# Kernel tuning notes

Measured on AMD Instinct MI355X. Metric: run time of the kernel, lower is better.

Reference implementation:

```python
import jax, jax.numpy as jnp
import numpy as np

HID = 1024
HEADS = 16
HEAD_DIM = HID // HEADS


def setup_inputs() -> dict:
    key = jax.random.key(0)
    ks = jax.random.split(key, 12)
    B, S = 4, 2048
    scale = 0.02
    return {
        "query": jax.random.normal(ks[0], (B, S, HID), jnp.float32),
        "key": jax.random.normal(ks[1], (B, S, HID), jnp.float32),
        "value": jax.random.normal(ks[2], (B, S, HID), jnp.float32),
        "wq": jax.random.normal(ks[3], (HID, HID), jnp.float32) * scale,
        "bq": jnp.zeros((HID,), jnp.float32),
        "wk": jax.random.normal(ks[4], (HID, HID), jnp.float32) * scale,
        "bk": jnp.zeros((HID,), jnp.float32),
        "wv": jax.random.normal(ks[5], (HID, HID), jnp.float32) * scale,
        "bv": jnp.zeros((HID,), jnp.float32),
        "wf": jax.random.normal(ks[6], (HID, HID), jnp.float32) * scale,
        "bf": jnp.zeros((HID,), jnp.float32),
    }


def reference(query, key, value, wq, bq, wk, bk, wv, bv, wf, bf):
    B, S, _ = query.shape
    # torch Linear: y = x @ W.T + b
    Q = (query @ wq.T + bq).reshape(B, S, HEADS, HEAD_DIM).transpose(0, 2, 1, 3)
    K = (key @ wk.T + bk).reshape(B, S, HEADS, HEAD_DIM).transpose(0, 2, 1, 3)
    V = (value @ wv.T + bv).reshape(B, S, HEADS, HEAD_DIM).transpose(0, 2, 1, 3)
    scale = jnp.sqrt(jnp.float32(HEAD_DIM))
    energy = jnp.einsum('bhqd,bhkd->bhqk', Q, K) / scale  # [B,H,S,S]
    attention = jax.nn.softmax(energy, axis=-1)  # dropout p=0 -> identity
    x = jnp.einsum('bhqk,bhkd->bhqd', attention, V)
    x = x.transpose(0, 2, 1, 3).reshape(B, S, HID)
    return x @ wf.T + bf
```

## Files before the change

kernel.cpp:

```cpp
#include <hip/hip_runtime.h>
#include <stdint.h>

#define SEQ 2048
#define HIDDEN 1024
#define NHEADS 16
#define HDIM 64
#define MTOT 8192

#define C1SCALE 0.1803368801111437f

typedef __bf16 bf16x8 __attribute__((ext_vector_type(8)));
typedef unsigned short u16x8 __attribute__((ext_vector_type(8)));
typedef short s16x4 __attribute__((ext_vector_type(4)));
typedef unsigned int u32x4 __attribute__((ext_vector_type(4)));
typedef float f32x4 __attribute__((ext_vector_type(4)));

#define GAS __attribute__((address_space(1)))
#define LAS __attribute__((address_space(3)))

__device__ __forceinline__ unsigned short bf16_rne(float f) {
  union { float f; unsigned int u; } v; v.f = f;
  return (unsigned short)((v.u + 0x7fffu + ((v.u >> 16) & 1u)) >> 16);
}

__device__ __forceinline__ unsigned int pk2(float lo, float hi) {
  unsigned int a = __builtin_bit_cast(unsigned int, hi) + 0x8000u;
  unsigned int b = __builtin_bit_cast(unsigned int, lo) + 0x8000u;
  return __builtin_amdgcn_perm(a, b, 0x07060302u);
}

__device__ __forceinline__ s16x4 pack4_bf16(float a, float b, float c, float d) {
  s16x4 r;
  r[0] = (short)bf16_rne(a); r[1] = (short)bf16_rne(b);
  r[2] = (short)bf16_rne(c); r[3] = (short)bf16_rne(d);
  return r;
}

__device__ __forceinline__ void gload_lds16(const unsigned short* g, unsigned short* l) {
  __builtin_amdgcn_global_load_lds((GAS void*)(unsigned short*)g, (LAS void*)l, 16, 0, 0);
}

__global__ __launch_bounds__(256) void cvt3(const float* __restrict__ a,
                                            const float* __restrict__ b,
                                            const float* __restrict__ c,
                                            unsigned short* __restrict__ out,
                                            int perSeg) {
  const int seg = blockIdx.y;
  const float* in = seg == 0 ? a : (seg == 1 ? b : c);
  int i = blockIdx.x * 256 + threadIdx.x;
  float4 v = ((const float4*)in)[i];
  ushort4 o;
  o.x = bf16_rne(v.x); o.y = bf16_rne(v.y);
  o.z = bf16_rne(v.z); o.w = bf16_rne(v.w);
  ((ushort4*)(out + (size_t)seg * perSeg))[i] = o;
}

__global__ __launch_bounds__(256) void cvt4(const float* __restrict__ a,
                                            const float* __restrict__ b,
                                            const float* __restrict__ c,
                                            const float* __restrict__ d,
                                            unsigned short* __restrict__ out,
                                            int perSeg) {
  const int seg = blockIdx.y;
  const float* in = seg == 0 ? a : (seg == 1 ? b : (seg == 2 ? c : d));
  const float sc = (seg == 0) ? C1SCALE : 1.0f;
  int i = blockIdx.x * 256 + threadIdx.x;
  float4 v = ((const float4*)in)[i];
  ushort4 o;
  o.x = bf16_rne(v.x * sc); o.y = bf16_rne(v.y * sc);
  o.z = bf16_rne(v.z * sc); o.w = bf16_rne(v.w * sc);
  ((ushort4*)(out + (size_t)seg * perSeg))[i] = o;
}

__global__ __launch_bounds__(256) void gemm_qkv(const unsigned short* __restrict__ Xq,
                                                const unsigned short* __restrict__ Xk,
                                                const unsigned short* __restrict__ Xv,
                                                const unsigned short* __restrict__ W,
                                                const float* __restrict__ bq,
                                                const float* __restrict__ bk,
                                                const float* __restrict__ bv,
                                                unsigned short* __restrict__ Qb,
                                                unsigned short* __restrict__ Kb,
                                                unsigned short* __restrict__ Vb) {
  __shared__ unsigned short As[128 * 32];
  __shared__ unsigned short Bs[128 * 32];
  const int tid = threadIdx.x;
  const int lane = tid & 63, w = tid >> 6;
  const int quad = lane >> 4, ln = lane & 15;
  const int wm = w & 1, wn = w >> 1;
  const int mBase = blockIdx.y * 128, nBase = blockIdx.x * 128;
  const int seg = blockIdx.x >> 3;
  const unsigned short* A = seg == 0 ? Xq : (seg == 1 ? Xk : Xv);
  const float* bias = seg == 0 ? bq : (seg == 1 ? bk : bv);
  const float bscale = seg == 0 ? C1SCALE : 1.0f;
  unsigned short* outp = seg == 0 ? Qb : (seg == 1 ? Kb : Vb);
  const int K = HIDDEN;

  f32x4 acc[4][4];
  f32x4 zero = {0.f, 0.f, 0.f, 0.f};
#pragma unroll
  for (int i = 0; i < 4; i++)
#pragma unroll
    for (int j = 0; j < 4; j++) acc[i][j] = zero;

  const int e0 = tid * 8;
  const int e1 = (256 + tid) * 8;
  const int r0 = e0 >> 5, c0 = e0 & 31;
  const int r1 = e1 >> 5, c1 = e1 & 31;
  const unsigned short* Ap0 = A + (size_t)(mBase + r0) * K + c0;
  const unsigned short* Ap1 = A + (size_t)(mBase + r1) * K + c1;
  const unsigned short* Wp0 = W + (size_t)(nBase + r0) * K + c0;
  const unsigned short* Wp1 = W + (size_t)(nBase + r1) * K + c1;

  for (int k0 = 0; k0 < K; k0 += 32) {
    gload_lds16(Ap0 + k0, &As[e0]);
    gload_lds16(Ap1 + k0, &As[e1]);
    gload_lds16(Wp0 + k0, &Bs[e0]);
    gload_lds16(Wp1 + k0, &Bs[e1]);
    __syncthreads();
    u16x8 af[4], bfr[4];
#pragma unroll
    for (int mi = 0; mi < 4; mi++)
      af[mi] = *(const u16x8*)&As[(wm * 64 + mi * 16 + ln) * 32 + quad * 8];
#pragma unroll
    for (int ni = 0; ni < 4; ni++)
      bfr[ni] = *(const u16x8*)&Bs[(wn * 64 + ni * 16 + ln) * 32 + quad * 8];
#pragma unroll
    for (int mi = 0; mi < 4; mi++)
#pragma unroll
      for (int ni = 0; ni < 4; ni++)
        acc[mi][ni] = __builtin_amdgcn_mfma_f32_16x16x32_bf16(
            __builtin_bit_cast(bf16x8, af[mi]), __builtin_bit_cast(bf16x8, bfr[ni]),
            acc[mi][ni], 0, 0, 0);
    __syncthreads();
  }

#pragma unroll
  for (int ni = 0; ni < 4; ni++) {
    const int colg = nBase + wn * 64 + ni * 16 + ln;
    const int col = colg & 1023;
    const float bvv = bias[col] * bscale;
#pragma unroll
    for (int mi = 0; mi < 4; mi++) {
      const int row = mBase + wm * 64 + mi * 16 + quad * 4;
#pragma unroll
      for (int r = 0; r < 4; r++)
        outp[(size_t)(row + r) * HIDDEN + col] = bf16_rne(acc[mi][ni][r] + bvv);
    }
  }
}

__global__ __launch_bounds__(256) void gemm_f(const unsigned short* __restrict__ A,
                                              const unsigned short* __restrict__ W,
                                              const float* __restrict__ bias,
                                              float* __restrict__ Cv) {
  __shared__ unsigned short As[128 * 32];
  __shared__ unsigned short Bs[128 * 32];
  const int tid = threadIdx.x;
  const int lane = tid & 63, w = tid >> 6;
  const int quad = lane >> 4, ln = lane & 15;
  const int wm = w & 1, wn = w >> 1;
  const int mBase = blockIdx.y * 128, nBase = blockIdx.x * 128;
  const int K = HIDDEN, N = HIDDEN;

  f32x4 acc[4][4];
  f32x4 zero = {0.f, 0.f, 0.f, 0.f};
#pragma unroll
  for (int i = 0; i < 4; i++)
#pragma unroll
    for (int j = 0; j < 4; j++) acc[i][j] = zero;

  const int e0 = tid * 8;
  const int e1 = (256 + tid) * 8;
  const int r0 = e0 >> 5, c0 = e0 & 31;
  const int r1 = e1 >> 5, c1 = e1 & 31;
  const unsigned short* Ap0 = A + (size_t)(mBase + r0) * K + c0;
  const unsigned short* Ap1 = A + (size_t)(mBase + r1) * K + c1;
  const unsigned short* Wp0 = W + (size_t)(nBase + r0) * K + c0;
  const unsigned short* Wp1 = W + (size_t)(nBase + r1) * K + c1;

  for (int k0 = 0; k0 < K; k0 += 32) {
    gload_lds16(Ap0 + k0, &As[e0]);
    gload_lds16(Ap1 + k0, &As[e1]);
    gload_lds16(Wp0 + k0, &Bs[e0]);
    gload_lds16(Wp1 + k0, &Bs[e1]);
    __syncthreads();
    u16x8 af[4], bfr[4];
#pragma unroll
    for (int mi = 0; mi < 4; mi++)
      af[mi] = *(const u16x8*)&As[(wm * 64 + mi * 16 + ln) * 32 + quad * 8];
#pragma unroll
    for (int ni = 0; ni < 4; ni++)
      bfr[ni] = *(const u16x8*)&Bs[(wn * 64 + ni * 16 + ln) * 32 + quad * 8];
#pragma unroll
    for (int mi = 0; mi < 4; mi++)
#pragma unroll
      for (int ni = 0; ni < 4; ni++)
        acc[mi][ni] = __builtin_amdgcn_mfma_f32_16x16x32_bf16(
            __builtin_bit_cast(bf16x8, af[mi]), __builtin_bit_cast(bf16x8, bfr[ni]),
            acc[mi][ni], 0, 0, 0);
    __syncthreads();
  }

#pragma unroll
  for (int ni = 0; ni < 4; ni++) {
    const int col = nBase + wn * 64 + ni * 16 + ln;
    const float bvv = bias[col];
#pragma unroll
    for (int mi = 0; mi < 4; mi++) {
      const int row = mBase + wm * 64 + mi * 16 + quad * 4;
#pragma unroll
      for (int r = 0; r < 4; r++)
        Cv[(size_t)(row + r) * N + col] = acc[mi][ni][r] + bvv;
    }
  }
}

__global__ __launch_bounds__(256) void transpose_v(const unsigned short* __restrict__ Vb,
                                                   unsigned short* __restrict__ Vt) {
  __shared__ unsigned short L[128 * 88];
  const int t = blockIdx.x;
  const int bh = t >> 4, kt = t & 15;
  const int b = bh >> 4, h = bh & 15;
  const int tid = threadIdx.x;
  {
    const int key = tid >> 1, hf = tid & 1;
    const unsigned short* src =
        Vb + ((size_t)(b * SEQ + kt * 128 + key)) * HIDDEN + h * HDIM + hf * 32;
    u16x8 a0 = *(const u16x8*)(src);
    u16x8 a1 = *(const u16x8*)(src + 8);
    u16x8 a2 = *(const u16x8*)(src + 16);
    u16x8 a3 = *(const u16x8*)(src + 24);
    unsigned short* dst = &L[key * 88 + hf * 32];
    *(u16x8*)(dst) = a0;
    *(u16x8*)(dst + 8) = a1;
    *(u16x8*)(dst + 16) = a2;
    *(u16x8*)(dst + 24) = a3;
  }
  __syncthreads();
  const int d = tid & 63, w = tid >> 6;
  unsigned short* out = Vt + (size_t)t * (64 * 128);
#pragma unroll
  for (int gg = 0; gg < 4; gg++) {
    const int G = w * 4 + gg;
    const int g = G >> 2, Phi = G & 3;
    u16x8 v;
#pragma unroll
    for (int j = 0; j < 8; j++) {
      const int kk = g * 32 + (j >> 2) * 16 + Phi * 4 + (j & 3);
      v[j] = L[kk * 88 + d];
    }
    *(u16x8*)(out + d * 128 + ((G ^ (d & 15)) * 8)) = v;
  }
}

__global__ __launch_bounds__(256, 3) void attn5(const unsigned short* __restrict__ Q,
                                                const unsigned short* __restrict__ K,
                                                const unsigned short* __restrict__ Vt,
                                                unsigned short* __restrict__ X) {
  __shared__ unsigned short VtL[2][64 * 128];
  const int tid = threadIdx.x, lane = tid & 63, w = tid >> 6;
  const int quad = lane >> 4, ln = lane & 15;
  const int bh = blockIdx.x, b = bh >> 4, h = bh & 15;
  const size_t base = (size_t)b * SEQ * HIDDEN + (size_t)h * HDIM;
  const unsigned short* Qh = Q + base;
  const unsigned short* Kh = K + base;
  const int qw = blockIdx.y * 128 + w * 32;

  u16x8 qf[2][2];
#pragma unroll
  for (int nt = 0; nt < 2; nt++)
#pragma unroll
    for (int kk2 = 0; kk2 < 2; kk2++)
      qf[nt][kk2] = *(const u16x8*)(Qh + (size_t)(qw + nt * 16 + ln) * HIDDEN + kk2 * 32 + quad * 8);

  f32x4 o[4][2];
  f32x4 zero = {0.f, 0.f, 0.f, 0.f};
#pragma unroll
  for (int mtd = 0; mtd < 4; mtd++)
#pragma unroll
    for (int nt = 0; nt < 2; nt++) o[mtd][nt] = zero;
  f32x4 lacc[2] = {zero, zero};

  const unsigned short* vsrc = Vt + (size_t)bh * 16 * (64 * 128);
  const int ldsOff = w * 2048 + lane * 8;
  const unsigned short* Kl = Kh + (size_t)ln * HIDDEN + quad * 8;

  u16x8 kp[4][2];
#pragma unroll
  for (int m = 0; m < 4; m++) {
    const size_t koff = (size_t)(m * 16) * HIDDEN;
    kp[m][0] = *(const u16x8*)(Kl + koff);
    kp[m][1] = *(const u16x8*)(Kl + koff + 32);
  }
#pragma unroll
  for (int i = 0; i < 4; i++)
    gload_lds16(vsrc + ldsOff + i * 512, &VtL[0][ldsOff + i * 512]);

  for (int kt = 0; kt < 16; ++kt) {
    __syncthreads();
    if (kt < 15) {
      const unsigned short* nsrc = vsrc + (size_t)(kt + 1) * (64 * 128);
      unsigned short* nbuf = &VtL[(kt + 1) & 1][0];
#pragma unroll
      for (int i = 0; i < 4; i++)
        gload_lds16(nsrc + ldsOff + i * 512, &nbuf[ldsOff + i * 512]);
    }
    const unsigned short* vb = &VtL[kt & 1][0];
#pragma unroll
    for (int g = 0; g < 4; g++) {
      u32x4 P[2];
#pragma unroll
      for (int half = 0; half < 2; half++) {
        const int mt = 2 * g + half;
        const int slot = mt & 3;
        f32x4 s0 = zero, s1 = zero;
        s0 = __builtin_amdgcn_mfma_f32_16x16x32_bf16(
            __builtin_bit_cast(bf16x8, kp[slot][0]), __builtin_bit_cast(bf16x8, qf[0][0]), s0, 0, 0, 0);
        s0 = __builtin_amdgcn_mfma_f32_16x16x32_bf16(
            __builtin_bit_cast(bf16x8, kp[slot][1]), __builtin_bit_cast(bf16x8, qf[0][1]), s0, 0, 0, 0);
        s1 = __builtin_amdgcn_mfma_f32_16x16x32_bf16(
            __builtin_bit_cast(bf16x8, kp[slot][0]), __builtin_bit_cast(bf16x8, qf[1][0]), s1, 0, 0, 0);
        s1 = __builtin_amdgcn_mfma_f32_16x16x32_bf16(
            __builtin_bit_cast(bf16x8, kp[slot][1]), __builtin_bit_cast(bf16x8, qf[1][1]), s1, 0, 0, 0);
        if (mt < 4) {
          const size_t koff = ((size_t)(kt * 128 + (mt + 4) * 16)) * HIDDEN;
          kp[slot][0] = *(const u16x8*)(Kl + koff);
          kp[slot][1] = *(const u16x8*)(Kl + koff + 32);
        } else if (kt < 15) {
          const size_t koff = ((size_t)((kt + 1) * 128 + (mt - 4) * 16)) * HIDDEN;
          kp[slot][0] = *(const u16x8*)(Kl + koff);
          kp[slot][1] = *(const u16x8*)(Kl + koff + 32);
        }
        float e0[4], e1[4];
#pragma unroll
        for (int r = 0; r < 4; r++) {
          e0[r] = __builtin_exp2f(s0[r]);
          e1[r] = __builtin_exp2f(s1[r]);
          lacc[0][r] += e0[r];
          lacc[1][r] += e1[r];
        }
        if (half == 0) {
          P[0][0] = pk2(e0[0], e0[1]); P[0][1] = pk2(e0[2], e0[3]);
          P[1][0] = pk2(e1[0], e1[1]); P[1][1] = pk2(e1[2], e1[3]);
        } else {
          P[0][2] = pk2(e0[0], e0[1]); P[0][3] = pk2(e0[2], e0[3]);
          P[1][2] = pk2(e1[0], e1[1]); P[1][3] = pk2(e1[2], e1[3]);
        }
      }
      u16x8 vf[4];
#pragma unroll
      for (int mtd = 0; mtd < 4; mtd++)
        vf[mtd] = *(const u16x8*)&vb[(mtd * 16 + ln) * 128 + (((g * 4 + quad) ^ ln) * 8)];
#pragma unroll
      for (int nt = 0; nt < 2; nt++) {
        bf16x8 pb = __builtin_bit_cast(bf16x8, P[nt]);
#pragma unroll
        for (int mtd = 0; mtd < 4; mtd++)
          o[mtd][nt] = __builtin_amdgcn_mfma_f32_16x16x32_bf16(
              __builtin_bit_cast(bf16x8, vf[mtd]), pb, o[mtd][nt], 0, 0, 0);
      }
    }
  }

  float inv[2];
#pragma unroll
  for (int nt = 0; nt < 2; nt++) {
    float l = lacc[nt][0] + lacc[nt][1] + lacc[nt][2] + lacc[nt][3];
    l += __shfl_xor(l, 16);
    l += __shfl_xor(l, 32);
    inv[nt] = 1.0f / l;
  }
#pragma unroll
  for (int nt = 0; nt < 2; nt++) {
    unsigned short* dst = X + (size_t)(b * SEQ + qw + nt * 16 + ln) * HIDDEN + h * HDIM;
#pragma unroll
    for (int mtd = 0; mtd < 4; mtd++) {
      s16x4 ov = pack4_bf16(o[mtd][nt][0] * inv[nt], o[mtd][nt][1] * inv[nt],
                            o[mtd][nt][2] * inv[nt], o[mtd][nt][3] * inv[nt]);
      *(s16x4*)(dst + mtd * 16 + quad * 4) = ov;
    }
  }
}

extern "C" void kernel_launch(void* const* d_in, const int* in_sizes, int n_in,
                              void* d_out, int out_size, void* d_ws, size_t ws_size,
                              hipStream_t stream) {
  const float* q_in = (const float*)d_in[0];
  const float* k_in = (const float*)d_in[1];
  const float* v_in = (const float*)d_in[2];
  const float* wq = (const float*)d_in[3];
  const float* bq = (const float*)d_in[4];
  const float* wk = (const float*)d_in[5];
  const float* bk = (const float*)d_in[6];
  const float* wv = (const float*)d_in[7];
  const float* bv = (const float*)d_in[8];
  const float* wf = (const float*)d_in[9];
  const float* bfb = (const float*)d_in[10];

  const size_t NX = (size_t)MTOT * HIDDEN;
  const size_t NW = (size_t)HIDDEN * HIDDEN;
  unsigned short* A = (unsigned short*)d_ws;
  unsigned short* Bx = A + NX;
  unsigned short* C = Bx + NX;
  unsigned short* W4 = C + NX;
  unsigned short* Qb = W4 + 4 * NW;
  unsigned short* Kb = Qb + NX;
  unsigned short* Vb = Kb + NX;

  cvt3<<<dim3(NX / 1024, 3), 256, 0, stream>>>(q_in, k_in, v_in, A, (int)NX);
  cvt4<<<dim3(NW / 1024, 4), 256, 0, stream>>>(wq, wk, wv, wf, W4, (int)NW);

  gemm_qkv<<<dim3(24, MTOT / 128), 256, 0, stream>>>(A, Bx, C, W4, bq, bk, bv, Qb, Kb, Vb);
  transpose_v<<<1024, 256, 0, stream>>>(Vb, Bx);
  attn5<<<dim3(NHEADS * 4, SEQ / 128), 256, 0, stream>>>(Qb, Kb, Bx, C);
  gemm_f<<<dim3(8, MTOT / 128), 256, 0, stream>>>(C, W4 + 3 * NW, bfb, (float*)d_out);
}
```

Measured before the change: 411.6 us.

## Pre-swizzle V into MFMA fragment order and load directly from global in attention

The transpose kernel now writes V in exact per-lane MFMA fragment order, so the attention kernel loads V operands straight from global memory and drops the LDS double buffer and its per-tile barriers. The row-sum of exponentials is computed by an extra MFMA against a ones vector instead of VALU adds and cross-lane shuffles. The K prefetch depth is cut from four slots to two, occupancy hint is raised to 4 blocks, and s_setprio brackets the MFMA sections. This trades LDS traffic and synchronisation for more global/L2 loads and one extra MFMA per group.

```diff
diff --git a/kernel.cpp b/kernel.cpp
--- a/kernel.cpp
+++ b/kernel.cpp
@@ -218,7 +218,7 @@
 
 __global__ __launch_bounds__(256) void transpose_v(const unsigned short* __restrict__ Vb,
                                                    unsigned short* __restrict__ Vt) {
-  __shared__ unsigned short L[128 * 88];
+  __shared__ unsigned short L[128 * 90];
   const int t = blockIdx.x;
   const int bh = t >> 4, kt = t & 15;
   const int b = bh >> 4, h = bh & 15;
@@ -231,40 +231,41 @@
     u16x8 a1 = *(const u16x8*)(src + 8);
     u16x8 a2 = *(const u16x8*)(src + 16);
     u16x8 a3 = *(const u16x8*)(src + 24);
-    unsigned short* dst = &L[key * 88 + hf * 32];
+    unsigned short* dst = &L[key * 90 + hf * 32];
     *(u16x8*)(dst) = a0;
     *(u16x8*)(dst + 8) = a1;
     *(u16x8*)(dst + 16) = a2;
     *(u16x8*)(dst + 24) = a3;
   }
   __syncthreads();
-  const int d = tid & 63, w = tid >> 6;
-  unsigned short* out = Vt + (size_t)t * (64 * 128);
+  const int lane = tid & 63, w = tid >> 6;
+  const int quad = lane >> 4, ln = lane & 15;
+  unsigned short* out = Vt + (size_t)t * 8192;
 #pragma unroll
   for (int gg = 0; gg < 4; gg++) {
-    const int G = w * 4 + gg;
-    const int g = G >> 2, Phi = G & 3;
+    const int f = w * 4 + gg;
+    const int g = f >> 2, mtd = f & 3;
     u16x8 v;
 #pragma unroll
     for (int j = 0; j < 8; j++) {
-      const int kk = g * 32 + (j >> 2) * 16 + Phi * 4 + (j & 3);
-      v[j] = L[kk * 88 + d];
+      const int key = g * 32 + (j >> 2) * 16 + quad * 4 + (j & 3);
+      v[j] = L[key * 90 + mtd * 16 + ln];
     }
-    *(u16x8*)(out + d * 128 + ((G ^ (d & 15)) * 8)) = v;
-  }
-}
-
-__global__ __launch_bounds__(256, 3) void attn5(const unsigned short* __restrict__ Q,
+    *(u16x8*)(out + f * 512 + lane * 8) = v;
+  }
+}
+
+__global__ __launch_bounds__(256, 4) void attn6(const unsigned short* __restrict__ Q,
                                                 const unsigned short* __restrict__ K,
                                                 const unsigned short* __restrict__ Vt,
                                                 unsigned short* __restrict__ X) {
-  __shared__ unsigned short VtL[2][64 * 128];
   const int tid = threadIdx.x, lane = tid & 63, w = tid >> 6;
   const int quad = lane >> 4, ln = lane & 15;
   const int bh = blockIdx.x, b = bh >> 4, h = bh & 15;
   const size_t base = (size_t)b * SEQ * HIDDEN + (size_t)h * HDIM;
   const unsigned short* Qh = Q + base;
   const unsigned short* Kh = K + base;
+  const unsigned short* vtile = Vt + (size_t)bh * 16 * 8192;
   const int qw = blockIdx.y * 128 + w * 32;
 
   u16x8 qf[2][2];
@@ -280,41 +281,35 @@
   for (int mtd = 0; mtd < 4; mtd++)
 #pragma unroll
     for (int nt = 0; nt < 2; nt++) o[mtd][nt] = zero;
-  f32x4 lacc[2] = {zero, zero};
-
-  const unsigned short* vsrc = Vt + (size_t)bh * 16 * (64 * 128);
-  const int ldsOff = w * 2048 + lane * 8;
+  f32x4 l2[2] = {zero, zero};
+
+  u16x8 onesf;
+#pragma unroll
+  for (int j = 0; j < 8; j++) onesf[j] = 0x3F80;
+
   const unsigned short* Kl = Kh + (size_t)ln * HIDDEN + quad * 8;
 
-  u16x8 kp[4][2];
-#pragma unroll
-  for (int m = 0; m < 4; m++) {
-    const size_t koff = (size_t)(m * 16) * HIDDEN;
-    kp[m][0] = *(const u16x8*)(Kl + koff);
-    kp[m][1] = *(const u16x8*)(Kl + koff + 32);
-  }
-#pragma unroll
-  for (int i = 0; i < 4; i++)
-    gload_lds16(vsrc + ldsOff + i * 512, &VtL[0][ldsOff + i * 512]);
+  u16x8 kp[2][2];
+  kp[0][0] = *(const u16x8*)(Kl);
+  kp[0][1] = *(const u16x8*)(Kl + 32);
+  kp[1][0] = *(const u16x8*)(Kl + 16 * HIDDEN);
+  kp[1][1] = *(const u16x8*)(Kl + 16 * HIDDEN + 32);
 
   for (int kt = 0; kt < 16; ++kt) {
-    __syncthreads();
-    if (kt < 15) {
-      const unsigned short* nsrc = vsrc + (size_t)(kt + 1) * (64 * 128);
-      unsigned short* nbuf = &VtL[(kt + 1) & 1][0];
-#pragma unroll
-      for (int i = 0; i < 4; i++)
-        gload_lds16(nsrc + ldsOff + i * 512, &nbuf[ldsOff + i * 512]);
-    }
-    const unsigned short* vb = &VtL[kt & 1][0];
 #pragma unroll
     for (int g = 0; g < 4; g++) {
+      u16x8 vp[4];
+#pragma unroll
+      for (int mtd = 0; mtd < 4; mtd++)
+        vp[mtd] = *(const u16x8*)(vtile + kt * 8192 + (g * 4 + mtd) * 512 + lane * 8);
+
       u32x4 P[2];
 #pragma unroll
       for (int half = 0; half < 2; half++) {
         const int mt = 2 * g + half;
-        const int slot = mt & 3;
+        const int slot = mt & 1;
         f32x4 s0 = zero, s1 = zero;
+        __builtin_amdgcn_s_setprio(1);
         s0 = __builtin_amdgcn_mfma_f32_16x16x32_bf16(
             __builtin_bit_cast(bf16x8, kp[slot][0]), __builtin_bit_cast(bf16x8, qf[0][0]), s0, 0, 0, 0);
         s0 = __builtin_amdgcn_mfma_f32_16x16x32_bf16(
@@ -323,22 +318,18 @@
             __builtin_bit_cast(bf16x8, kp[slot][0]), __builtin_bit_cast(bf16x8, qf[1][0]), s1, 0, 0, 0);
         s1 = __builtin_amdgcn_mfma_f32_16x16x32_bf16(
             __builtin_bit_cast(bf16x8, kp[slot][1]), __builtin_bit_cast(bf16x8, qf[1][1]), s1, 0, 0, 0);
-        if (mt < 4) {
-          const size_t koff = ((size_t)(kt * 128 + (mt + 4) * 16)) * HIDDEN;
-          kp[slot][0] = *(const u16x8*)(Kl + koff);
-          kp[slot][1] = *(const u16x8*)(Kl + koff + 32);
-        } else if (kt < 15) {
-          const size_t koff = ((size_t)((kt + 1) * 128 + (mt - 4) * 16)) * HIDDEN;
-          kp[slot][0] = *(const u16x8*)(Kl + koff);
-          kp[slot][1] = *(const u16x8*)(Kl + koff + 32);
+        __builtin_amdgcn_s_setprio(0);
+        const int nxt = kt * 8 + mt + 2;
+        if (nxt < 128) {
+          const unsigned short* ka = Kl + (size_t)nxt * 16 * HIDDEN;
+          kp[slot][0] = *(const u16x8*)(ka);
+          kp[slot][1] = *(const u16x8*)(ka + 32);
         }
         float e0[4], e1[4];
 #pragma unroll
         for (int r = 0; r < 4; r++) {
           e0[r] = __builtin_exp2f(s0[r]);
           e1[r] = __builtin_exp2f(s1[r]);
-          lacc[0][r] += e0[r];
-          lacc[1][r] += e1[r];
         }
         if (half == 0) {
           P[0][0] = pk2(e0[0], e0[1]); P[0][1] = pk2(e0[2], e0[3]);
@@ -348,29 +339,25 @@
           P[1][2] = pk2(e1[0], e1[1]); P[1][3] = pk2(e1[2], e1[3]);
         }
       }
-      u16x8 vf[4];
-#pragma unroll
-      for (int mtd = 0; mtd < 4; mtd++)
-        vf[mtd] = *(const u16x8*)&vb[(mtd * 16 + ln) * 128 + (((g * 4 + quad) ^ ln) * 8)];
+      __builtin_amdgcn_s_setprio(1);
 #pragma unroll
       for (int nt = 0; nt < 2; nt++) {
         bf16x8 pb = __builtin_bit_cast(bf16x8, P[nt]);
+        l2[nt] = __builtin_amdgcn_mfma_f32_16x16x32_bf16(
+            __builtin_bit_cast(bf16x8, onesf), pb, l2[nt], 0, 0, 0);
 #pragma unroll
         for (int mtd = 0; mtd < 4; mtd++)
           o[mtd][nt] = __builtin_amdgcn_mfma_f32_16x16x32_bf16(
-              __builtin_bit_cast(bf16x8, vf[mtd]), pb, o[mtd][nt], 0, 0, 0);
+              __builtin_bit_cast(bf16x8, vp[mtd]), pb, o[mtd][nt], 0, 0, 0);
       }
+      __builtin_amdgcn_s_setprio(0);
     }
   }
 
   float inv[2];
 #pragma unroll
-  for (int nt = 0; nt < 2; nt++) {
-    float l = lacc[nt][0] + lacc[nt][1] + lacc[nt][2] + lacc[nt][3];
-    l += __shfl_xor(l, 16);
-    l += __shfl_xor(l, 32);
-    inv[nt] = 1.0f / l;
-  }
+  for (int nt = 0; nt < 2; nt++) inv[nt] = 1.0f / l2[nt][0];
+
 #pragma unroll
   for (int nt = 0; nt < 2; nt++) {
     unsigned short* dst = X + (size_t)(b * SEQ + qw + nt * 16 + ln) * HIDDEN + h * HDIM;
@@ -413,6 +400,6 @@
 
   gemm_qkv<<<dim3(24, MTOT / 128), 256, 0, stream>>>(A, Bx, C, W4, bq, bk, bv, Qb, Kb, Vb);
   transpose_v<<<1024, 256, 0, stream>>>(Vb, Bx);
-  attn5<<<dim3(NHEADS * 4, SEQ / 128), 256, 0, stream>>>(Qb, Kb, Bx, C);
+  attn6<<<dim3(NHEADS * 4, SEQ / 128), 256, 0, stream>>>(Qb, Kb, Bx, C);
   gemm_f<<<dim3(8, MTOT / 128), 256, 0, stream>>>(C, W4 + 3 * NW, bfb, (float*)d_out);
 }
```

Measured after the change: 431.3 us. 1.05x slower.
